# Performance work log

Hardware: AMD Instinct MI355X
Metric: run time of the kernel (lower is better)

## Reference

```python
import jax, jax.numpy as jnp
import numpy as np
import math

D_MODEL = 1024
NUM_HEADS = 16
HEAD_DIM = D_MODEL // NUM_HEADS
BATCH = 2
SEQ = 2048
NEG_INF = -1000000.0  # matches torch code's -1e6 fill


def setup_inputs() -> dict:
    key = jax.random.key(0)
    ks = jax.random.split(key, 10)
    s = 1.0 / math.sqrt(D_MODEL)
    inp = {
        "X": jax.random.normal(ks[0], (BATCH, SEQ, D_MODEL), dtype=jnp.float32),
        "Wq": jax.random.uniform(ks[1], (D_MODEL, D_MODEL), minval=-s, maxval=s, dtype=jnp.float32),
        "bq": jnp.zeros((D_MODEL,), jnp.float32),
        "Wk": jax.random.uniform(ks[2], (D_MODEL, D_MODEL), minval=-s, maxval=s, dtype=jnp.float32),
        "bk": jnp.zeros((D_MODEL,), jnp.float32),
        "Wv": jax.random.uniform(ks[3], (D_MODEL, D_MODEL), minval=-s, maxval=s, dtype=jnp.float32),
        "bv": jnp.zeros((D_MODEL,), jnp.float32),
        "Wo": jax.random.uniform(ks[4], (D_MODEL, D_MODEL), minval=-s, maxval=s, dtype=jnp.float32),
        "bo": jnp.zeros((D_MODEL,), jnp.float32),
        "valid_lens": jax.random.randint(ks[5], (BATCH, NUM_HEADS), 1, SEQ + 1, dtype=jnp.int64)
        if jax.config.jax_enable_x64 else
        jax.random.randint(ks[5], (BATCH, NUM_HEADS), 1, SEQ + 1, dtype=jnp.int32),
    }
    return inp


def _split_heads(Y, B, S):
    # (B, S, D) -> (B*H, S, head_dim), matching transpose_qkv
    return Y.reshape(B, S, NUM_HEADS, HEAD_DIM).transpose(0, 2, 1, 3).reshape(B * NUM_HEADS, S, HEAD_DIM)


def reference(X, Wq, bq, Wk, bk, Wv, bv, Wo, bo, valid_lens):
    B, S, D = X.shape
    q = _split_heads(X @ Wq.T + bq, B, S)
    k = _split_heads(X @ Wk.T + bk, B, S)
    v = _split_heads(X @ Wv.T + bv, B, S)
    scores = jnp.einsum("bqd,bkd->bqk", q, k) / math.sqrt(HEAD_DIM)  # (B*H, S, S)
    # Faithful to torch code: 2-D valid_lens reshaped to (B*H,), mask over
    # the first two dims -> entire query rows j >= valid_len set to -1e6.
    row_mask = jnp.arange(S)[None, :] < valid_lens.reshape(-1)[:, None]  # (B*H, S)
    scores = jnp.where(row_mask[:, :, None], scores, NEG_INF)
    attn = jax.nn.softmax(scores, axis=-1)
    out = jnp.einsum("bqk,bkd->bqd", attn, v)  # (B*H, S, head_dim)
    out = out.reshape(B, NUM_HEADS, S, HEAD_DIM).transpose(0, 2, 1, 3).reshape(B, S, D)
    return out @ Wo.T + bo
```

## Files before the change

### kernel.cpp

```cpp
#include <hip/hip_runtime.h>

#define SQ 2048
#define DM 1024
#define NH 16
#define HD 64

typedef __bf16 bf16x8 __attribute__((ext_vector_type(8)));
typedef float f32x4 __attribute__((ext_vector_type(4)));
typedef unsigned short u16;
typedef unsigned int u32;

__device__ __forceinline__ u16 f2b(float f) {
  union { float f; u32 u; } c; c.f = f;
  return (u16)((c.u + 0x7FFFu + ((c.u >> 16) & 1u)) >> 16);
}

__device__ __forceinline__ void gll16(const void* g, void* l) {
  __builtin_amdgcn_global_load_lds(
      (const __attribute__((address_space(1))) void*)g,
      (__attribute__((address_space(3))) void*)l, 16, 0, 0);
}

__global__ void __launch_bounds__(256) conv_bf16(
    const float* __restrict__ X,
    const float* __restrict__ Wq, const float* __restrict__ Wk,
    const float* __restrict__ Wv, const float* __restrict__ Wo,
    u16* __restrict__ Xb, u16* __restrict__ Wqb, u16* __restrict__ Wkb,
    u16* __restrict__ Wvb, u16* __restrict__ Wob) {
  const size_t e = ((size_t)blockIdx.x * 256 + threadIdx.x) * 8;
  const float* src; u16* dst; size_t rel;
  if (e < 4194304u)      { src = X;  dst = Xb;  rel = e; }
  else if (e < 5242880u) { src = Wq; dst = Wqb; rel = e - 4194304u; }
  else if (e < 6291456u) { src = Wk; dst = Wkb; rel = e - 5242880u; }
  else if (e < 7340032u) { src = Wv; dst = Wvb; rel = e - 6291456u; }
  else                   { src = Wo; dst = Wob; rel = e - 7340032u; }
  float4 a = *(const float4*)(src + rel);
  float4 b = *(const float4*)(src + rel + 4);
  union { u16 h[8]; uint4 v; } o;
  o.h[0] = f2b(a.x); o.h[1] = f2b(a.y); o.h[2] = f2b(a.z); o.h[3] = f2b(a.w);
  o.h[4] = f2b(b.x); o.h[5] = f2b(b.y); o.h[6] = f2b(b.z); o.h[7] = f2b(b.w);
  *(uint4*)(dst + rel) = o.v;
}

__global__ void __launch_bounds__(256) mean_v(
    const u16* __restrict__ Vt, u16* __restrict__ mv) {
  __shared__ float part[256];
  const int bh = blockIdx.x;
  const int t = threadIdx.x, d = t >> 2, c = t & 3;
  const u16* row = Vt + ((size_t)bh * HD + d) * SQ + c * 512;
  float s = 0.f;
  for (int i = 0; i < 64; ++i) {
    bf16x8 v = *(const bf16x8*)(row + i * 8);
    s += ((float)v[0] + (float)v[1]) + ((float)v[2] + (float)v[3])
       + ((float)v[4] + (float)v[5]) + ((float)v[6] + (float)v[7]);
  }
  part[t] = s;
  __syncthreads();
  if (c == 0) {
    const float tot = (part[t] + part[t + 1]) + (part[t + 2] + part[t + 3]);
    mv[bh * HD + d] = f2b(tot * (1.0f / 2048.0f));
  }
}

__device__ __forceinline__ void stage128(const u16* __restrict__ A, const u16* __restrict__ B,
                                         u16* sA, u16* sB, int m0, int n0, int kt,
                                         int w, int l) {
#pragma unroll
  for (int c = 0; c < 2; ++c) {
    const int g = w * 2 + c;
    const int s = g * 64 + l;
    const int r = s >> 2, cc = s & 3;
    gll16(A + (size_t)(m0 + r) * DM + kt * 32 + cc * 8, sA + g * 512);
    gll16(B + (size_t)(n0 + r) * DM + kt * 32 + cc * 8, sB + g * 512);
  }
}

__device__ __forceinline__ void gemm_core2(const u16* __restrict__ A, const u16* __restrict__ B,
                                           u16* sA, u16* sB,
                                           int m0, int n0, f32x4 acc[4][4]) {
  const int t = threadIdx.x, l = t & 63, w = t >> 6;
  const int wr = w >> 1, wc = w & 1, lg = l >> 4, li = l & 15;

  stage128(A, B, sA, sB, m0, n0, 0, w, l);
  __syncthreads();
  int cur = 0;
  for (int kt = 0; kt < DM / 32; ++kt) {
    if (kt + 1 < DM / 32)
      stage128(A, B, sA + (cur ^ 1) * 4096, sB + (cur ^ 1) * 4096, m0, n0, kt + 1, w, l);
    bf16x8 aF[4], bF[4];
#pragma unroll
    for (int mi = 0; mi < 4; ++mi)
      aF[mi] = *(const bf16x8*)(sA + cur * 4096 + (wr * 64 + mi * 16 + li) * 32 + lg * 8);
#pragma unroll
    for (int ni = 0; ni < 4; ++ni)
      bF[ni] = *(const bf16x8*)(sB + cur * 4096 + (wc * 64 + ni * 16 + li) * 32 + lg * 8);
#pragma unroll
    for (int mi = 0; mi < 4; ++mi)
#pragma unroll
      for (int ni = 0; ni < 4; ++ni)
        acc[mi][ni] = __builtin_amdgcn_mfma_f32_16x16x32_bf16(aF[mi], bF[ni], acc[mi][ni], 0, 0, 0);
    __syncthreads();
    cur ^= 1;
  }
}

__global__ void __launch_bounds__(256) qkv_gemm(
    const u16* __restrict__ Xb, const u16* __restrict__ Wqkv,
    const float* __restrict__ bq, const float* __restrict__ bk, const float* __restrict__ bv,
    u16* __restrict__ Qb, u16* __restrict__ Kb, u16* __restrict__ Vt) {
  __shared__ u16 sA[8192];
  __shared__ u16 sB[8192];
  const int id = blockIdx.x;
  const int swz = (id & 7) * 96 + (id >> 3);
  const int bx = swz % 24, by = swz / 24;
  const int m0 = by * 128, n0 = bx * 128;
  const int mode = n0 >> 10;
  const float* bias = (mode == 0) ? bq : (mode == 1) ? bk : bv;

  f32x4 acc[4][4];
  f32x4 z4 = {0.f, 0.f, 0.f, 0.f};
#pragma unroll
  for (int i = 0; i < 4; ++i)
#pragma unroll
    for (int j = 0; j < 4; ++j) acc[i][j] = z4;

  gemm_core2(Xb, Wqkv, sA, sB, m0, n0, acc);

  const int t = threadIdx.x;
  const int l = t & 63, w = t >> 6;
  const int wr = w >> 1, wc = w & 1, lg = l >> 4, li = l & 15;
#pragma unroll
  for (int mi = 0; mi < 4; ++mi) {
    const int m = m0 + wr * 64 + mi * 16 + lg * 4;
    const int b = m >> 11;
    const int s = m & 2047;
#pragma unroll
    for (int ni = 0; ni < 4; ++ni) {
      const int n = n0 + wc * 64 + ni * 16 + li;
      const int nn = n - (mode << 10);
      const int h = nn >> 6, dd = nn & 63;
      const float bia = bias[nn];
      const size_t bh = (size_t)(b * NH + h);
      if (mode == 2) {
        union { u16 h4[4]; uint2 u; } pk;
#pragma unroll
        for (int r = 0; r < 4; ++r) pk.h4[r] = f2b(acc[mi][ni][r] + bia);
        *(uint2*)(Vt + (bh * HD + dd) * SQ + s) = pk.u;
      } else {
#pragma unroll
        for (int r = 0; r < 4; ++r) {
          const float val = acc[mi][ni][r] + bia;
          const int ss = s + r;
          if (mode == 0) Qb[(bh * SQ + ss) * HD + dd] = f2b(val * 0.180336880f);
          else           Kb[(bh * SQ + ss) * HD + dd] = f2b(val);
        }
      }
    }
  }
}

__global__ void __launch_bounds__(256) out_gemm(
    const u16* __restrict__ Ag, const u16* __restrict__ Wob,
    const float* __restrict__ bo, float* __restrict__ out) {
  __shared__ u16 sA[2][2048];
  __shared__ u16 sB[2][4096];
  const int t = threadIdx.x, l = t & 63, w = t >> 6;
  const int wr = w >> 1, wc = w & 1, lg = l >> 4, li = l & 15;
  const int id = blockIdx.x;
  const int swz = (id & 7) * 64 + (id >> 3);
  const int bx = swz >> 6, by = swz & 63;
  const int m0 = by * 64, n0 = bx * 128;

  auto stage = [&](int buf, int kt) {
    {
      const int s = w * 64 + l;
      const int r = s >> 2, cc = s & 3;
      gll16(Ag + (size_t)(m0 + r) * DM + kt * 32 + cc * 8, &sA[buf][w * 512]);
    }
#pragma unroll
    for (int c = 0; c < 2; ++c) {
      const int g = w * 2 + c;
      const int s = g * 64 + l;
      const int r = s >> 2, cc = s & 3;
      gll16(Wob + (size_t)(n0 + r) * DM + kt * 32 + cc * 8, &sB[buf][g * 512]);
    }
  };

  f32x4 acc[2][4];
  f32x4 z4 = {0.f, 0.f, 0.f, 0.f};
#pragma unroll
  for (int i = 0; i < 2; ++i)
#pragma unroll
    for (int j = 0; j < 4; ++j) acc[i][j] = z4;

  stage(0, 0);
  __syncthreads();
  int cur = 0;
  for (int kt = 0; kt < DM / 32; ++kt) {
    if (kt + 1 < DM / 32) stage(cur ^ 1, kt + 1);
    bf16x8 aF[2], bF[4];
#pragma unroll
    for (int mi = 0; mi < 2; ++mi)
      aF[mi] = *(const bf16x8*)(&sA[cur][(wr * 32 + mi * 16 + li) * 32 + lg * 8]);
#pragma unroll
    for (int ni = 0; ni < 4; ++ni)
      bF[ni] = *(const bf16x8*)(&sB[cur][(wc * 64 + ni * 16 + li) * 32 + lg * 8]);
#pragma unroll
    for (int mi = 0; mi < 2; ++mi)
#pragma unroll
      for (int ni = 0; ni < 4; ++ni)
        acc[mi][ni] = __builtin_amdgcn_mfma_f32_16x16x32_bf16(aF[mi], bF[ni], acc[mi][ni], 0, 0, 0);
    __syncthreads();
    cur ^= 1;
  }

#pragma unroll
  for (int mi = 0; mi < 2; ++mi) {
    const int m = m0 + wr * 32 + mi * 16 + lg * 4;
#pragma unroll
    for (int ni = 0; ni < 4; ++ni) {
      const int n = n0 + wc * 64 + ni * 16 + li;
      const float bia = bo[n];
#pragma unroll
      for (int r = 0; r < 4; ++r)
        out[(size_t)(m + r) * DM + n] = acc[mi][ni][r] + bia;
    }
  }
}

__global__ void __launch_bounds__(256, 2) attn_v11(
    const u16* __restrict__ Qb, const u16* __restrict__ Kb, const u16* __restrict__ Vt,
    const int* __restrict__ vlen, const u16* __restrict__ mv, u16* __restrict__ Ao) {
  __shared__ u16 sKV[4][2][4096];
  __shared__ float lpart[4][4][16];
  const int bh = blockIdx.x, qt = blockIdx.y;
  const int t = threadIdx.x, w = t >> 6, l = t & 63, lg = l >> 4, li = l & 15;
  const int vl = vlen[bh];
  const int q0 = qt * 64;
  const int b = bh >> 4, h = bh & 15;

  if (q0 >= vl) {
    const size_t rowb = ((size_t)(b * SQ + q0 + w * 16 + li)) * DM + h * HD;
#pragma unroll
    for (int n2 = 0; n2 < 4; ++n2) {
      const uint2 v = *(const uint2*)(mv + bh * HD + n2 * 16 + lg * 4);
      *(uint2*)(Ao + rowb + n2 * 16 + lg * 4) = v;
    }
    return;
  }

  const u16* Qh = Qb + (size_t)bh * SQ * HD;
  const u16* Kh = Kb + (size_t)bh * SQ * HD;
  const u16* Vh = Vt + (size_t)bh * HD * SQ;
  const int k0 = w * 512;

  bf16x8 qf[4][2];
#pragma unroll
  for (int g = 0; g < 4; ++g) {
    const bool mq = (q0 + g * 16 + li) >= vl;
#pragma unroll
    for (int kk = 0; kk < 2; ++kk) {
      qf[g][kk] = *(const bf16x8*)(Qh + (size_t)(q0 + g * 16 + li) * HD + kk * 32 + lg * 8);
      if (mq) {
        union { u32 u[4]; bf16x8 v; } z; z.u[0] = z.u[1] = z.u[2] = z.u[3] = 0;
        qf[g][kk] = z.v;
      }
    }
  }

  union { u16 h[8]; bf16x8 v; } onesU;
#pragma unroll
  for (int j = 0; j < 8; ++j) onesU.h[j] = 0x3F80;
  const bf16x8 ones = onesU.v;

  int kOff[4], vOff[4];
#pragma unroll
  for (int i = 0; i < 4; ++i) {
    {
      const int s = i * 64 + l, row = s >> 3, c = s & 7;
      const int csrc = c ^ (row & 7);
      const int sig = (((row >> 2) & 3) << 3) | (((row >> 4) & 1) << 2) | (row & 3);
      kOff[i] = sig * HD + csrc * 8;
    }
    {
      const int s = i * 64 + l, d = s >> 2, c = s & 3;
      const int csrc = c ^ ((d >> 2) & 3);
      vOff[i] = d * SQ + csrc * 8;
    }
  }

  u16* sw = &sKV[w][0][0];
  auto stage = [&](int buf, int tt) {
    const u16* kb = Kh + (size_t)(k0 + tt * 32) * HD;
    const u16* vb = Vh + (size_t)(k0 + tt * 32);
    u16* db = sw + buf * 4096;
#pragma unroll
    for (int i = 0; i < 4; ++i) gll16(kb + kOff[i], db + i * 512);
#pragma unroll
    for (int i = 0; i < 4; ++i) gll16(vb + vOff[i], db + 2048 + i * 512);
  };

  f32x4 z4 = {0.f, 0.f, 0.f, 0.f};
  f32x4 acc[4][4], lacc[4];
#pragma unroll
  for (int g = 0; g < 4; ++g) {
    lacc[g] = z4;
#pragma unroll
    for (int n2 = 0; n2 < 4; ++n2) acc[g][n2] = z4;
  }

  stage(0, 0);
  int cur = 0;
  for (int tt = 0; tt < 16; ++tt) {
    if (tt < 15) {
      stage(cur ^ 1, tt + 1);
      asm volatile("s_waitcnt vmcnt(8)" ::: "memory");
    } else {
      asm volatile("s_waitcnt vmcnt(0)" ::: "memory");
    }
    const u16* kb_ = sw + cur * 4096;
    const u16* vb_ = sw + cur * 4096 + 2048;

    bf16x8 kf[2][2], vf[4];
#pragma unroll
    for (int ni = 0; ni < 2; ++ni) {
      const int row = ni * 16 + li;
      kf[ni][0] = *(const bf16x8*)(kb_ + row * 64 + ((lg ^ (row & 7)) * 8));
      kf[ni][1] = *(const bf16x8*)(kb_ + row * 64 + (((4 + lg) ^ (row & 7)) * 8));
    }
#pragma unroll
    for (int n2 = 0; n2 < 4; ++n2) {
      const int d = n2 * 16 + li;
      vf[n2] = *(const bf16x8*)(vb_ + d * 32 + ((lg ^ ((d >> 2) & 3)) * 8));
    }

    __builtin_amdgcn_s_setprio(1);
#pragma unroll
    for (int g = 0; g < 4; ++g) {
      f32x4 s0 = __builtin_amdgcn_mfma_f32_16x16x32_bf16(kf[0][0], qf[g][0], z4, 0, 0, 0);
      s0 = __builtin_amdgcn_mfma_f32_16x16x32_bf16(kf[0][1], qf[g][1], s0, 0, 0, 0);
      f32x4 s1 = __builtin_amdgcn_mfma_f32_16x16x32_bf16(kf[1][0], qf[g][0], z4, 0, 0, 0);
      s1 = __builtin_amdgcn_mfma_f32_16x16x32_bf16(kf[1][1], qf[g][1], s1, 0, 0, 0);

      union { __bf16 e[8]; bf16x8 v; } P;
#pragma unroll
      for (int r = 0; r < 4; ++r) {
        P.e[r]     = (__bf16)__builtin_amdgcn_exp2f(s0[r]);
        P.e[4 + r] = (__bf16)__builtin_amdgcn_exp2f(s1[r]);
      }

      lacc[g] = __builtin_amdgcn_mfma_f32_16x16x32_bf16(ones, P.v, lacc[g], 0, 0, 0);
#pragma unroll
      for (int n2 = 0; n2 < 4; ++n2)
        acc[g][n2] = __builtin_amdgcn_mfma_f32_16x16x32_bf16(vf[n2], P.v, acc[g][n2], 0, 0, 0);
    }
    __builtin_amdgcn_s_setprio(0);
    cur ^= 1;
  }

  __syncthreads();
  f32x4* op = (f32x4*)&sKV[0][0][0];
#pragma unroll
  for (int g = 0; g < 4; ++g) {
#pragma unroll
    for (int n2 = 0; n2 < 4; ++n2)
      op[(((w * 4) + g) * 4 + n2) * 64 + l] = acc[g][n2];
    if (lg == 0) lpart[w][g][li] = lacc[g][0];
  }
  __syncthreads();

  const int g = w;
  const float lf = lpart[0][g][li] + lpart[1][g][li] + lpart[2][g][li] + lpart[3][g][li];
  const float inv = 1.0f / lf;
  const size_t rowb = ((size_t)(b * SQ + q0 + g * 16 + li)) * DM + h * HD;
#pragma unroll
  for (int n2 = 0; n2 < 4; ++n2) {
    f32x4 s = op[((0 * 4 + g) * 4 + n2) * 64 + l];
    s += op[((1 * 4 + g) * 4 + n2) * 64 + l];
    s += op[((2 * 4 + g) * 4 + n2) * 64 + l];
    s += op[((3 * 4 + g) * 4 + n2) * 64 + l];
    union { __bf16 h2[4]; uint2 u; } ov;
#pragma unroll
    for (int r = 0; r < 4; ++r) ov.h2[r] = (__bf16)(s[r] * inv);
    *(uint2*)(Ao + rowb + n2 * 16 + lg * 4) = ov.u;
  }
}

extern "C" void kernel_launch(void* const* d_in, const int* in_sizes, int n_in,
                              void* d_out, int out_size, void* d_ws, size_t ws_size,
                              hipStream_t stream) {
  const float* X  = (const float*)d_in[0];
  const float* Wq = (const float*)d_in[1];
  const float* bq = (const float*)d_in[2];
  const float* Wk = (const float*)d_in[3];
  const float* bk = (const float*)d_in[4];
  const float* Wv = (const float*)d_in[5];
  const float* bv = (const float*)d_in[6];
  const float* Wo = (const float*)d_in[7];
  const float* bo = (const float*)d_in[8];
  const int* vlen = (const int*)d_in[9];

  char* ws = (char*)d_ws;
  u16* Qb  = (u16*)(ws);
  u16* Kb  = (u16*)(ws + (size_t)8388608);
  u16* Vt  = (u16*)(ws + (size_t)16777216);
  u16* Xb  = (u16*)(ws + (size_t)25165824);
  u16* Ao  = Xb;
  u16* Wqb = (u16*)(ws + (size_t)33554432);
  u16* Wkb = (u16*)(ws + (size_t)35651584);
  u16* Wvb = (u16*)(ws + (size_t)37748736);
  u16* Wob = (u16*)(ws + (size_t)39845888);

  u16* mv = (u16*)d_out;

  dim3 blk(256);
  conv_bf16<<<4096, blk, 0, stream>>>(X, Wq, Wk, Wv, Wo, Xb, Wqb, Wkb, Wvb, Wob);
  qkv_gemm<<<768, blk, 0, stream>>>(Xb, Wqb, bq, bk, bv, Qb, Kb, Vt);
  mean_v<<<32, blk, 0, stream>>>(Vt, mv);
  attn_v11<<<dim3(32, 32), blk, 0, stream>>>(Qb, Kb, Vt, vlen, mv, Ao);
  out_gemm<<<512, blk, 0, stream>>>(Ao, Wob, bo, (float*)d_out);
}
```

Before: 124.1 us.

## Rewrite QKV GEMM with 256x256 tiles, triple-buffered LDS, and masked Q skip

Replaces the 128x128 QKV GEMM with a 512-thread kernel that computes 256x256 tiles. It uses a three-stage LDS pipeline with explicit vmcnt waits, an XOR swizzle to avoid bank conflicts, and split MFMA phases with raised wave priority. Blocks whose Q rows lie past every covered head's valid length return early, since those query rows are fully masked. The out_gemm block swizzle is dropped for a plain 2D grid. The larger tile gives more reuse per block but launches only 192 blocks, fewer than the CU count, which risks underfilling the GPU.

```diff
diff --git a/kernel.cpp b/kernel.cpp
--- a/kernel.cpp
+++ b/kernel.cpp
@@ -62,94 +62,129 @@
   }
 }
 
-__device__ __forceinline__ void stage128(const u16* __restrict__ A, const u16* __restrict__ B,
-                                         u16* sA, u16* sB, int m0, int n0, int kt,
-                                         int w, int l) {
-#pragma unroll
-  for (int c = 0; c < 2; ++c) {
-    const int g = w * 2 + c;
-    const int s = g * 64 + l;
-    const int r = s >> 2, cc = s & 3;
-    gll16(A + (size_t)(m0 + r) * DM + kt * 32 + cc * 8, sA + g * 512);
-    gll16(B + (size_t)(n0 + r) * DM + kt * 32 + cc * 8, sB + g * 512);
-  }
-}
-
-__device__ __forceinline__ void gemm_core2(const u16* __restrict__ A, const u16* __restrict__ B,
-                                           u16* sA, u16* sB,
-                                           int m0, int n0, f32x4 acc[4][4]) {
-  const int t = threadIdx.x, l = t & 63, w = t >> 6;
-  const int wr = w >> 1, wc = w & 1, lg = l >> 4, li = l & 15;
-
-  stage128(A, B, sA, sB, m0, n0, 0, w, l);
-  __syncthreads();
-  int cur = 0;
-  for (int kt = 0; kt < DM / 32; ++kt) {
-    if (kt + 1 < DM / 32)
-      stage128(A, B, sA + (cur ^ 1) * 4096, sB + (cur ^ 1) * 4096, m0, n0, kt + 1, w, l);
-    bf16x8 aF[4], bF[4];
-#pragma unroll
-    for (int mi = 0; mi < 4; ++mi)
-      aF[mi] = *(const bf16x8*)(sA + cur * 4096 + (wr * 64 + mi * 16 + li) * 32 + lg * 8);
-#pragma unroll
-    for (int ni = 0; ni < 4; ++ni)
-      bF[ni] = *(const bf16x8*)(sB + cur * 4096 + (wc * 64 + ni * 16 + li) * 32 + lg * 8);
-#pragma unroll
-    for (int mi = 0; mi < 4; ++mi)
-#pragma unroll
-      for (int ni = 0; ni < 4; ++ni)
-        acc[mi][ni] = __builtin_amdgcn_mfma_f32_16x16x32_bf16(aF[mi], bF[ni], acc[mi][ni], 0, 0, 0);
-    __syncthreads();
-    cur ^= 1;
-  }
-}
-
-__global__ void __launch_bounds__(256) qkv_gemm(
+__global__ void __launch_bounds__(512, 1) qkv_gemm8(
     const u16* __restrict__ Xb, const u16* __restrict__ Wqkv,
     const float* __restrict__ bq, const float* __restrict__ bk, const float* __restrict__ bv,
+    const int* __restrict__ vlen,
     u16* __restrict__ Qb, u16* __restrict__ Kb, u16* __restrict__ Vt) {
-  __shared__ u16 sA[8192];
-  __shared__ u16 sB[8192];
+  __shared__ u16 lds[3 * 16384];
+  const int tid = threadIdx.x, w = tid >> 6, l = tid & 63, lg = l >> 4, li = l & 15;
+  const int wm = w >> 2, wn = w & 3;
+
   const int id = blockIdx.x;
-  const int swz = (id & 7) * 96 + (id >> 3);
-  const int bx = swz % 24, by = swz / 24;
-  const int m0 = by * 128, n0 = bx * 128;
+  const int swz = (id & 7) * 24 + (id >> 3);
+  const int bx = swz % 12, by = swz / 12;
+  const int m0 = by * 256, n0 = bx * 256;
   const int mode = n0 >> 10;
   const float* bias = (mode == 0) ? bq : (mode == 1) ? bk : bv;
 
-  f32x4 acc[4][4];
+  if (mode == 0) {
+    const int bb = m0 >> 11, s0 = m0 & 2047, h0 = n0 >> 6;
+    if (s0 >= vlen[bb * NH + h0]     && s0 >= vlen[bb * NH + h0 + 1] &&
+        s0 >= vlen[bb * NH + h0 + 2] && s0 >= vlen[bb * NH + h0 + 3]) return;
+  }
+
+  int srcOff[2];
+#pragma unroll
+  for (int j = 0; j < 2; ++j) {
+    const int c = w * 2 + j;
+    const int row = c * 16 + (l >> 2);
+    const int colsrc = ((l & 3) * 8) ^ (((row >> 3) & 1) << 4);
+    srcOff[j] = row * DM + colsrc;
+  }
+  const u16* Abase = Xb + (size_t)m0 * DM;
+  const u16* Bbase = Wqkv + (size_t)n0 * DM;
+
+  auto stage = [&](int buf, int kt) {
+    u16* db = lds + buf * 16384;
+#pragma unroll
+    for (int j = 0; j < 2; ++j)
+      gll16(Abase + srcOff[j] + kt * 32, db + (w * 2 + j) * 512);
+#pragma unroll
+    for (int j = 0; j < 2; ++j)
+      gll16(Bbase + srcOff[j] + kt * 32, db + 8192 + (w * 2 + j) * 512);
+  };
+
+  f32x4 acc[8][4];
   f32x4 z4 = {0.f, 0.f, 0.f, 0.f};
 #pragma unroll
-  for (int i = 0; i < 4; ++i)
+  for (int i = 0; i < 8; ++i)
 #pragma unroll
     for (int j = 0; j < 4; ++j) acc[i][j] = z4;
 
-  gemm_core2(Xb, Wqkv, sA, sB, m0, n0, acc);
-
-  const int t = threadIdx.x;
-  const int l = t & 63, w = t >> 6;
-  const int wr = w >> 1, wc = w & 1, lg = l >> 4, li = l & 15;
-#pragma unroll
-  for (int mi = 0; mi < 4; ++mi) {
-    const int m = m0 + wr * 64 + mi * 16 + lg * 4;
+  stage(0, 0);
+  stage(1, 1);
+
+  for (int t = 0; t < 32; ++t) {
+    const int bsel = t % 3;
+    if (t + 2 < 32) stage((t + 2) % 3, t + 2);
+    if (t < 30)      asm volatile("s_waitcnt vmcnt(8)" ::: "memory");
+    else if (t == 30) asm volatile("s_waitcnt vmcnt(4)" ::: "memory");
+    else              asm volatile("s_waitcnt vmcnt(0)" ::: "memory");
+    __builtin_amdgcn_s_barrier();
+    asm volatile("" ::: "memory");
+
+    const u16* A_ = lds + bsel * 16384;
+    const u16* B_ = A_ + 8192;
+
+    bf16x8 aF[8];
+#pragma unroll
+    for (int fm = 0; fm < 8; ++fm) {
+      const int rl = wm * 128 + fm * 16 + li;
+      aF[fm] = *(const bf16x8*)(A_ + rl * 32 + ((lg * 8) ^ (((rl >> 3) & 1) << 4)));
+    }
+    {
+      const int r0 = wn * 64 + 0 * 16 + li, r1 = wn * 64 + 1 * 16 + li;
+      bf16x8 b0 = *(const bf16x8*)(B_ + r0 * 32 + ((lg * 8) ^ (((r0 >> 3) & 1) << 4)));
+      bf16x8 b1 = *(const bf16x8*)(B_ + r1 * 32 + ((lg * 8) ^ (((r1 >> 3) & 1) << 4)));
+      __builtin_amdgcn_s_setprio(1);
+#pragma unroll
+      for (int fm = 0; fm < 8; ++fm) {
+        acc[fm][0] = __builtin_amdgcn_mfma_f32_16x16x32_bf16(aF[fm], b0, acc[fm][0], 0, 0, 0);
+        acc[fm][1] = __builtin_amdgcn_mfma_f32_16x16x32_bf16(aF[fm], b1, acc[fm][1], 0, 0, 0);
+      }
+      __builtin_amdgcn_s_setprio(0);
+    }
+    __builtin_amdgcn_s_barrier();
+    asm volatile("" ::: "memory");
+    {
+      const int r2 = wn * 64 + 2 * 16 + li, r3 = wn * 64 + 3 * 16 + li;
+      bf16x8 b2 = *(const bf16x8*)(B_ + r2 * 32 + ((lg * 8) ^ (((r2 >> 3) & 1) << 4)));
+      bf16x8 b3 = *(const bf16x8*)(B_ + r3 * 32 + ((lg * 8) ^ (((r3 >> 3) & 1) << 4)));
+      __builtin_amdgcn_s_setprio(1);
+#pragma unroll
+      for (int fm = 0; fm < 8; ++fm) {
+        acc[fm][2] = __builtin_amdgcn_mfma_f32_16x16x32_bf16(aF[fm], b2, acc[fm][2], 0, 0, 0);
+        acc[fm][3] = __builtin_amdgcn_mfma_f32_16x16x32_bf16(aF[fm], b3, acc[fm][3], 0, 0, 0);
+      }
+      __builtin_amdgcn_s_setprio(0);
+    }
+    asm volatile("" ::: "memory");
+    __builtin_amdgcn_s_barrier();
+    asm volatile("" ::: "memory");
+  }
+
+#pragma unroll
+  for (int fm = 0; fm < 8; ++fm) {
+    const int m = m0 + wm * 128 + fm * 16 + lg * 4;
     const int b = m >> 11;
     const int s = m & 2047;
 #pragma unroll
-    for (int ni = 0; ni < 4; ++ni) {
-      const int n = n0 + wc * 64 + ni * 16 + li;
-      const int nn = n - (mode << 10);
+    for (int fn = 0; fn < 4; ++fn) {
+      const int n = n0 + wn * 64 + fn * 16 + li;
+      const int nn = n & 1023;
       const int h = nn >> 6, dd = nn & 63;
       const float bia = bias[nn];
       const size_t bh = (size_t)(b * NH + h);
       if (mode == 2) {
         union { u16 h4[4]; uint2 u; } pk;
 #pragma unroll
-        for (int r = 0; r < 4; ++r) pk.h4[r] = f2b(acc[mi][ni][r] + bia);
+        for (int r = 0; r < 4; ++r) pk.h4[r] = f2b(acc[fm][fn][r] + bia);
         *(uint2*)(Vt + (bh * HD + dd) * SQ + s) = pk.u;
       } else {
 #pragma unroll
         for (int r = 0; r < 4; ++r) {
-          const float val = acc[mi][ni][r] + bia;
+          const float val = acc[fm][fn][r] + bia;
           const int ss = s + r;
           if (mode == 0) Qb[(bh * SQ + ss) * HD + dd] = f2b(val * 0.180336880f);
           else           Kb[(bh * SQ + ss) * HD + dd] = f2b(val);
@@ -166,10 +201,7 @@
   __shared__ u16 sB[2][4096];
   const int t = threadIdx.x, l = t & 63, w = t >> 6;
   const int wr = w >> 1, wc = w & 1, lg = l >> 4, li = l & 15;
-  const int id = blockIdx.x;
-  const int swz = (id & 7) * 64 + (id >> 3);
-  const int bx = swz >> 6, by = swz & 63;
-  const int m0 = by * 64, n0 = bx * 128;
+  const int m0 = blockIdx.y * 64, n0 = blockIdx.x * 128;
 
   auto stage = [&](int buf, int kt) {
     {
@@ -415,8 +447,8 @@
 
   dim3 blk(256);
   conv_bf16<<<4096, blk, 0, stream>>>(X, Wq, Wk, Wv, Wo, Xb, Wqb, Wkb, Wvb, Wob);
-  qkv_gemm<<<768, blk, 0, stream>>>(Xb, Wqb, bq, bk, bv, Qb, Kb, Vt);
+  qkv_gemm8<<<192, dim3(512), 0, stream>>>(Xb, Wqb, bq, bk, bv, vlen, Qb, Kb, Vt);
   mean_v<<<32, blk, 0, stream>>>(Vt, mv);
   attn_v11<<<dim3(32, 32), blk, 0, stream>>>(Qb, Kb, Vt, vlen, mv, Ao);
-  out_gemm<<<512, blk, 0, stream>>>(Ao, Wob, bo, (float*)d_out);
-}
+  out_gemm<<<dim3(8, 64), blk, 0, stream>>>(Ao, Wob, bo, (float*)d_out);
+}
```

After: 124.7 us. About the same (+0.5%).
